# Kernel tuning notes

Hardware: AMD Instinct MI355X
Metric: run time of the kernel (lower is better)

Reference implementation:

```python
import jax, jax.numpy as jnp
import numpy as np

N_ATOMS = 1_000_000
N_MOL = 50_000
NF = 128


def setup_inputs() -> dict:
    key = jax.random.key(0)
    ks = jax.random.split(key, 10)
    inp = {
        "charges": jax.random.normal(ks[0], (N_ATOMS, 1), dtype=jnp.float32),
        "f0": jax.random.normal(ks[1], (N_ATOMS, NF), dtype=jnp.float32),
        "f1": jax.random.normal(ks[2], (N_ATOMS, NF), dtype=jnp.float32),
        "f2": jax.random.normal(ks[3], (N_ATOMS, NF), dtype=jnp.float32),
        "mol_index": jnp.sort(jax.random.randint(ks[4], (N_ATOMS,), 0, N_MOL, dtype=jnp.int64) if jax.config.jax_enable_x64 else jax.random.randint(ks[4], (N_ATOMS,), 0, N_MOL).astype(jnp.int32)),
        "n_molecules": N_MOL,
        # Linear(nf, 1) params; first layer has bias=first_is_interacting=False.
        "w0": jax.random.normal(ks[5], (NF,), dtype=jnp.float32) / np.sqrt(NF),
        "w1": jax.random.normal(ks[6], (NF,), dtype=jnp.float32) / np.sqrt(NF),
        "w2": jax.random.normal(ks[7], (NF,), dtype=jnp.float32) / np.sqrt(NF),
        "b1": jax.random.normal(ks[8], (), dtype=jnp.float32) * 0.01,
        "b2": jax.random.normal(ks[9], (), dtype=jnp.float32) * 0.01,
    }
    return inp


def reference(charges, f0, f1, f2, mol_index, n_molecules, w0, w1, w2, b1, b2):
    # Per-term nf->1 projections, summed. [n_atoms, 1]
    total_lin = (f0 @ w0 + (f1 @ w1 + b1) + (f2 @ w2 + b2))[:, None]
    # Source bug (reproduced faithfully): quad terms also use layers_lin,
    # so total_quad == total_lin.
    total_quad = total_lin
    atom_charge_energy = (total_quad * charges) ** 2 + total_lin
    molecule_charge_energy = jax.ops.segment_sum(
        atom_charge_energy, mol_index, num_segments=n_molecules
    )
    return (molecule_charge_energy, atom_charge_energy)
```

## Files before the change

### kernel.cpp

```cpp
#include <hip/hip_runtime.h>


typedef float f32x4 __attribute__((ext_vector_type(4)));

__global__ void zero_kernel(float* __restrict__ p, int n) {
    int i = blockIdx.x * blockDim.x + threadIdx.x;
    if (i < n) p[i] = 0.0f;
}

__device__ __forceinline__ float dot12(const f32x4 a, const f32x4 b, const f32x4 c,
                                       const f32x4 wa, const f32x4 wb, const f32x4 wc) {
    return a.x * wa.x + a.y * wa.y + a.z * wa.z + a.w * wa.w
         + b.x * wb.x + b.y * wb.y + b.z * wb.z + b.w * wb.w
         + c.x * wc.x + c.y * wc.y + c.z * wc.z + c.w * wc.w;
}

__global__ void __launch_bounds__(256)
charge_energy_kernel(const float* __restrict__ charges,
                     const float* __restrict__ f0,
                     const float* __restrict__ f1,
                     const float* __restrict__ f2,
                     const int*   __restrict__ mol_index,
                     const float* __restrict__ w0,
                     const float* __restrict__ w1,
                     const float* __restrict__ w2,
                     const float* __restrict__ b1p,
                     const float* __restrict__ b2p,
                     float* __restrict__ mol_out,
                     float* __restrict__ atom_out,
                     int n_atoms,
                     int chunk)
{
    const int lane   = threadIdx.x & 63;
    const int lane32 = lane & 31;
    const long long wid = (long long)blockIdx.x * (blockDim.x >> 6) + (threadIdx.x >> 6);

    long long a0 = wid * (long long)chunk;
    if (a0 >= n_atoms) return;
    long long a1 = a0 + chunk;
    if (a1 > n_atoms) a1 = n_atoms;

    const float bias = b1p[0] + b2p[0];
    const f32x4 w0c = reinterpret_cast<const f32x4*>(w0)[lane32];
    const f32x4 w1c = reinterpret_cast<const f32x4*>(w1)[lane32];
    const f32x4 w2c = reinterpret_cast<const f32x4*>(w2)[lane32];

    int   cur_mol = -1;
    float cur_sum = 0.0f;

    long long a = a0;
    for (; a + 4 <= a1; a += 4) {
        const f32x4* p0 = reinterpret_cast<const f32x4*>(f0) + a * 32;
        const f32x4* p1 = reinterpret_cast<const f32x4*>(f1) + a * 32;
        const f32x4* p2 = reinterpret_cast<const f32x4*>(f2) + a * 32;

        const f32x4 xa0 = __builtin_nontemporal_load(p0 + lane);
        const f32x4 xa1 = __builtin_nontemporal_load(p1 + lane);
        const f32x4 xa2 = __builtin_nontemporal_load(p2 + lane);
        const f32x4 xb0 = __builtin_nontemporal_load(p0 + 64 + lane);
        const f32x4 xb1 = __builtin_nontemporal_load(p1 + 64 + lane);
        const f32x4 xb2 = __builtin_nontemporal_load(p2 + 64 + lane);

        const float4 cc = *reinterpret_cast<const float4*>(charges + a);
        const int4   mm = *reinterpret_cast<const int4*>(mol_index + a);

        float pA = dot12(xa0, xa1, xa2, w0c, w1c, w2c);
        float pB = dot12(xb0, xb1, xb2, w0c, w1c, w2c);

        #pragma unroll
        for (int m = 16; m >= 1; m >>= 1) {
            pA += __shfl_xor(pA, m, 64);
            pB += __shfl_xor(pB, m, 64);
        }
        const float s1 = __shfl(pA, 32, 64);
        const float s3 = __shfl(pB, 32, 64);

        if (lane == 0) {
            const float lin0 = pA + bias, lin1 = s1 + bias;
            const float lin2 = pB + bias, lin3 = s3 + bias;
            const float t0 = lin0 * cc.x, t1 = lin1 * cc.y;
            const float t2 = lin2 * cc.z, t3 = lin3 * cc.w;
            const float e0 = t0 * t0 + lin0, e1 = t1 * t1 + lin1;
            const float e2 = t2 * t2 + lin2, e3 = t3 * t3 + lin3;
            *reinterpret_cast<float4*>(atom_out + a) = make_float4(e0, e1, e2, e3);

            const int   ms[4] = {mm.x, mm.y, mm.z, mm.w};
            const float es[4] = {e0, e1, e2, e3};
            #pragma unroll
            for (int k = 0; k < 4; ++k) {
                if (ms[k] != cur_mol) {
                    if (cur_mol >= 0) atomicAdd(&mol_out[cur_mol], cur_sum);
                    cur_mol = ms[k]; cur_sum = es[k];
                } else {
                    cur_sum += es[k];
                }
            }
        }
    }
    if (a + 2 <= a1) {
        const f32x4 x0 = (reinterpret_cast<const f32x4*>(f0) + a * 32)[lane];
        const f32x4 x1 = (reinterpret_cast<const f32x4*>(f1) + a * 32)[lane];
        const f32x4 x2 = (reinterpret_cast<const f32x4*>(f2) + a * 32)[lane];
        const float2 cc = *reinterpret_cast<const float2*>(charges + a);
        const int2   mm = *reinterpret_cast<const int2*>(mol_index + a);
        float p = dot12(x0, x1, x2, w0c, w1c, w2c);
        #pragma unroll
        for (int m = 16; m >= 1; m >>= 1) p += __shfl_xor(p, m, 64);
        const float sB = __shfl(p, 32, 64);
        if (lane == 0) {
            const float lin0 = p + bias, lin1 = sB + bias;
            const float t0 = lin0 * cc.x, t1 = lin1 * cc.y;
            const float e0 = t0 * t0 + lin0, e1 = t1 * t1 + lin1;
            *reinterpret_cast<float2*>(atom_out + a) = make_float2(e0, e1);
            if (mm.x != cur_mol) {
                if (cur_mol >= 0) atomicAdd(&mol_out[cur_mol], cur_sum);
                cur_mol = mm.x; cur_sum = e0;
            } else cur_sum += e0;
            if (mm.y != cur_mol) {
                atomicAdd(&mol_out[cur_mol], cur_sum);
                cur_mol = mm.y; cur_sum = e1;
            } else cur_sum += e1;
        }
        a += 2;
    }
    if (a < a1) {
        const f32x4 x0 = (reinterpret_cast<const f32x4*>(f0) + a * 32)[lane32];
        const f32x4 x1 = (reinterpret_cast<const f32x4*>(f1) + a * 32)[lane32];
        const f32x4 x2 = (reinterpret_cast<const f32x4*>(f2) + a * 32)[lane32];
        float p = dot12(x0, x1, x2, w0c, w1c, w2c);
        #pragma unroll
        for (int m = 16; m >= 1; m >>= 1) p += __shfl_xor(p, m, 64);
        if (lane == 0) {
            const float lin = p + bias;
            const float t = lin * charges[a];
            const float e = t * t + lin;
            atom_out[a] = e;
            const int mi = mol_index[a];
            if (mi != cur_mol) {
                if (cur_mol >= 0) atomicAdd(&mol_out[cur_mol], cur_sum);
                cur_mol = mi; cur_sum = e;
            } else cur_sum += e;
        }
    }
    if (lane == 0 && cur_mol >= 0)
        atomicAdd(&mol_out[cur_mol], cur_sum);
}

extern "C" void kernel_launch(void* const* d_in, const int* in_sizes, int n_in,
                              void* d_out, int out_size, void* d_ws, size_t ws_size,
                              hipStream_t stream) {
    const float* charges   = (const float*)d_in[0];
    const float* f0        = (const float*)d_in[1];
    const float* f1        = (const float*)d_in[2];
    const float* f2        = (const float*)d_in[3];
    const int*   mol_index = (const int*)  d_in[4];
    const float* w0        = (const float*)d_in[6];
    const float* w1        = (const float*)d_in[7];
    const float* w2        = (const float*)d_in[8];
    const float* b1p       = (const float*)d_in[9];
    const float* b2p       = (const float*)d_in[10];

    const int n_atoms = in_sizes[0];
    const int n_mol   = out_size - n_atoms;

    float* mol_out  = (float*)d_out;
    float* atom_out = mol_out + n_mol;

    {
        int blocks = (n_mol + 255) / 256;
        hipLaunchKernelGGL(zero_kernel, dim3(blocks), dim3(256), 0, stream,
                           mol_out, n_mol);
    }

    const int blocks  = 2048;
    const int n_waves = blocks * (256 / 64);
    int chunk = (n_atoms + n_waves - 1) / n_waves;
    chunk = (chunk + 3) & ~3;

    hipLaunchKernelGGL(charge_energy_kernel, dim3(blocks), dim3(256), 0, stream,
                       charges, f0, f1, f2, mol_index, w0, w1, w2, b1p, b2p,
                       mol_out, atom_out, n_atoms, chunk);
}
```

Baseline: 268.3 us.

## Software-prefetch next atom quad and balance per-wave work partition

Each wave now loads the feature vectors for its next group of four atoms while computing the current group, double-buffering in registers. Work is split into quads distributed evenly across waves with a remainder, replacing the rounded fixed chunk that left some waves short or idle. The atom output store becomes nontemporal. The prefetch raises register pressure, which may reduce occupancy.

Result: slower. 277.9 us (+3.6%).

```diff
diff --git a/kernel.cpp b/kernel.cpp
--- a/kernel.cpp
+++ b/kernel.cpp
@@ -29,43 +29,61 @@
                      float* __restrict__ mol_out,
                      float* __restrict__ atom_out,
                      int n_atoms,
-                     int chunk)
+                     int nq_base,
+                     int nq_rem,
+                     int n_waves)
 {
     const int lane   = threadIdx.x & 63;
     const int lane32 = lane & 31;
     const long long wid = (long long)blockIdx.x * (blockDim.x >> 6) + (threadIdx.x >> 6);
+    if (wid >= n_waves) return;
 
-    long long a0 = wid * (long long)chunk;
-    if (a0 >= n_atoms) return;
-    long long a1 = a0 + chunk;
-    if (a1 > n_atoms) a1 = n_atoms;
+    const long long q0 = wid * (long long)nq_base + (wid < nq_rem ? wid : nq_rem);
+    const long long q1 = q0 + nq_base + (wid < nq_rem ? 1 : 0);
+    long long a  = q0 * 4;
+    const long long aQ = q1 * 4;
 
     const float bias = b1p[0] + b2p[0];
     const f32x4 w0c = reinterpret_cast<const f32x4*>(w0)[lane32];
     const f32x4 w1c = reinterpret_cast<const f32x4*>(w1)[lane32];
     const f32x4 w2c = reinterpret_cast<const f32x4*>(w2)[lane32];
 
+    const f32x4* p0 = reinterpret_cast<const f32x4*>(f0);
+    const f32x4* p1 = reinterpret_cast<const f32x4*>(f1);
+    const f32x4* p2 = reinterpret_cast<const f32x4*>(f2);
+
     int   cur_mol = -1;
     float cur_sum = 0.0f;
 
-    long long a = a0;
-    for (; a + 4 <= a1; a += 4) {
-        const f32x4* p0 = reinterpret_cast<const f32x4*>(f0) + a * 32;
-        const f32x4* p1 = reinterpret_cast<const f32x4*>(f1) + a * 32;
-        const f32x4* p2 = reinterpret_cast<const f32x4*>(f2) + a * 32;
+    f32x4 ca0, ca1, ca2, cb0, cb1, cb2;
+    if (a < aQ) {
+        const long long base = a * 32;
+        ca0 = __builtin_nontemporal_load(p0 + base + lane);
+        ca1 = __builtin_nontemporal_load(p1 + base + lane);
+        ca2 = __builtin_nontemporal_load(p2 + base + lane);
+        cb0 = __builtin_nontemporal_load(p0 + base + 64 + lane);
+        cb1 = __builtin_nontemporal_load(p1 + base + 64 + lane);
+        cb2 = __builtin_nontemporal_load(p2 + base + 64 + lane);
+    }
 
-        const f32x4 xa0 = __builtin_nontemporal_load(p0 + lane);
-        const f32x4 xa1 = __builtin_nontemporal_load(p1 + lane);
-        const f32x4 xa2 = __builtin_nontemporal_load(p2 + lane);
-        const f32x4 xb0 = __builtin_nontemporal_load(p0 + 64 + lane);
-        const f32x4 xb1 = __builtin_nontemporal_load(p1 + 64 + lane);
-        const f32x4 xb2 = __builtin_nontemporal_load(p2 + 64 + lane);
+    for (; a < aQ; a += 4) {
+        f32x4 na0, na1, na2, nb0, nb1, nb2;
+        const bool has_next = (a + 4 < aQ);
+        if (has_next) {
+            const long long nb = (a + 4) * 32;
+            na0 = __builtin_nontemporal_load(p0 + nb + lane);
+            na1 = __builtin_nontemporal_load(p1 + nb + lane);
+            na2 = __builtin_nontemporal_load(p2 + nb + lane);
+            nb0 = __builtin_nontemporal_load(p0 + nb + 64 + lane);
+            nb1 = __builtin_nontemporal_load(p1 + nb + 64 + lane);
+            nb2 = __builtin_nontemporal_load(p2 + nb + 64 + lane);
+        }
 
         const float4 cc = *reinterpret_cast<const float4*>(charges + a);
         const int4   mm = *reinterpret_cast<const int4*>(mol_index + a);
 
-        float pA = dot12(xa0, xa1, xa2, w0c, w1c, w2c);
-        float pB = dot12(xb0, xb1, xb2, w0c, w1c, w2c);
+        float pA = dot12(ca0, ca1, ca2, w0c, w1c, w2c);
+        float pB = dot12(cb0, cb1, cb2, w0c, w1c, w2c);
 
         #pragma unroll
         for (int m = 16; m >= 1; m >>= 1) {
@@ -82,7 +100,8 @@
             const float t2 = lin2 * cc.z, t3 = lin3 * cc.w;
             const float e0 = t0 * t0 + lin0, e1 = t1 * t1 + lin1;
             const float e2 = t2 * t2 + lin2, e3 = t3 * t3 + lin3;
-            *reinterpret_cast<float4*>(atom_out + a) = make_float4(e0, e1, e2, e3);
+            f32x4 ev; ev.x = e0; ev.y = e1; ev.z = e2; ev.w = e3;
+            __builtin_nontemporal_store(ev, reinterpret_cast<f32x4*>(atom_out + a));
 
             const int   ms[4] = {mm.x, mm.y, mm.z, mm.w};
             const float es[4] = {e0, e1, e2, e3};
@@ -96,52 +115,36 @@
                 }
             }
         }
-    }
-    if (a + 2 <= a1) {
-        const f32x4 x0 = (reinterpret_cast<const f32x4*>(f0) + a * 32)[lane];
-        const f32x4 x1 = (reinterpret_cast<const f32x4*>(f1) + a * 32)[lane];
-        const f32x4 x2 = (reinterpret_cast<const f32x4*>(f2) + a * 32)[lane];
-        const float2 cc = *reinterpret_cast<const float2*>(charges + a);
-        const int2   mm = *reinterpret_cast<const int2*>(mol_index + a);
-        float p = dot12(x0, x1, x2, w0c, w1c, w2c);
-        #pragma unroll
-        for (int m = 16; m >= 1; m >>= 1) p += __shfl_xor(p, m, 64);
-        const float sB = __shfl(p, 32, 64);
-        if (lane == 0) {
-            const float lin0 = p + bias, lin1 = sB + bias;
-            const float t0 = lin0 * cc.x, t1 = lin1 * cc.y;
-            const float e0 = t0 * t0 + lin0, e1 = t1 * t1 + lin1;
-            *reinterpret_cast<float2*>(atom_out + a) = make_float2(e0, e1);
-            if (mm.x != cur_mol) {
-                if (cur_mol >= 0) atomicAdd(&mol_out[cur_mol], cur_sum);
-                cur_mol = mm.x; cur_sum = e0;
-            } else cur_sum += e0;
-            if (mm.y != cur_mol) {
-                atomicAdd(&mol_out[cur_mol], cur_sum);
-                cur_mol = mm.y; cur_sum = e1;
-            } else cur_sum += e1;
-        }
-        a += 2;
-    }
-    if (a < a1) {
-        const f32x4 x0 = (reinterpret_cast<const f32x4*>(f0) + a * 32)[lane32];
-        const f32x4 x1 = (reinterpret_cast<const f32x4*>(f1) + a * 32)[lane32];
-        const f32x4 x2 = (reinterpret_cast<const f32x4*>(f2) + a * 32)[lane32];
-        float p = dot12(x0, x1, x2, w0c, w1c, w2c);
-        #pragma unroll
-        for (int m = 16; m >= 1; m >>= 1) p += __shfl_xor(p, m, 64);
-        if (lane == 0) {
-            const float lin = p + bias;
-            const float t = lin * charges[a];
-            const float e = t * t + lin;
-            atom_out[a] = e;
-            const int mi = mol_index[a];
-            if (mi != cur_mol) {
-                if (cur_mol >= 0) atomicAdd(&mol_out[cur_mol], cur_sum);
-                cur_mol = mi; cur_sum = e;
-            } else cur_sum += e;
+
+        if (has_next) {
+            ca0 = na0; ca1 = na1; ca2 = na2;
+            cb0 = nb0; cb1 = nb1; cb2 = nb2;
         }
     }
+
+    if (wid == n_waves - 1) {
+        for (long long r = aQ > (long long)(n_atoms & ~3LL) ? aQ : (long long)(n_atoms & ~3LL);
+             r < n_atoms; ++r) {
+            const f32x4 x0 = (p0 + r * 32)[lane32];
+            const f32x4 x1 = (p1 + r * 32)[lane32];
+            const f32x4 x2 = (p2 + r * 32)[lane32];
+            float p = dot12(x0, x1, x2, w0c, w1c, w2c);
+            #pragma unroll
+            for (int m = 16; m >= 1; m >>= 1) p += __shfl_xor(p, m, 64);
+            if (lane == 0) {
+                const float lin = p + bias;
+                const float t = lin * charges[r];
+                const float e = t * t + lin;
+                atom_out[r] = e;
+                const int mi = mol_index[r];
+                if (mi != cur_mol) {
+                    if (cur_mol >= 0) atomicAdd(&mol_out[cur_mol], cur_sum);
+                    cur_mol = mi; cur_sum = e;
+                } else cur_sum += e;
+            }
+        }
+    }
+
     if (lane == 0 && cur_mol >= 0)
         atomicAdd(&mol_out[cur_mol], cur_sum);
 }
@@ -174,10 +177,11 @@
 
     const int blocks  = 2048;
     const int n_waves = blocks * (256 / 64);
-    int chunk = (n_atoms + n_waves - 1) / n_waves;
-    chunk = (chunk + 3) & ~3;
+    const int nq      = n_atoms >> 2;
+    const int nq_base = nq / n_waves;
+    const int nq_rem  = nq % n_waves;
 
     hipLaunchKernelGGL(charge_energy_kernel, dim3(blocks), dim3(256), 0, stream,
                        charges, f0, f1, f2, mol_index, w0, w1, w2, b1p, b2p,
-                       mol_out, atom_out, n_atoms, chunk);
+                       mol_out, atom_out, n_atoms, nq_base, nq_rem, n_waves);
 }
```
